# Performance work log

Measured on AMD Instinct MI355X. Metric: run time of the kernel, lower is better.

Reference implementation:

```python
import jax, jax.numpy as jnp
import numpy as np

EPS = 1e-08

def _compute_W(V, C, eps=EPS):
    # W = H_k ... H_1, applied sequentially as in the torch loop
    W = jnp.eye(C, dtype=V.dtype)
    def step(W, v):
        v = v / (jnp.linalg.norm(v) + eps)
        # H @ W = W - 2 v (v^T W)
        W = W - 2.0 * jnp.outer(v, v @ W)
        return W, None
    W, _ = jax.lax.scan(step, W, V)
    return W

def setup_inputs() -> dict:
    key = jax.random.key(0)
    k1, k2 = jax.random.split(key)
    x = jax.random.normal(k1, (16, 512, 64, 64), dtype=jnp.float32)
    V = jax.random.normal(k2, (32, 512), dtype=jnp.float32)
    return {"x": x, "V": V}

def reference(x, V):
    B, C, H, Wd = x.shape
    W = _compute_W(V, C)  # [C, C] orthogonal
    # 1x1 conv: out[b,o,h,w] = sum_c W[o,c] * x[b,c,h,w]
    return jnp.einsum('oc,bchw->bohw', W, x)
```

## Files before the change

### kernel.cpp

```cpp
#include <hip/hip_runtime.h>
#include <hip/hip_bf16.h>
#include <stdint.h>
#include <stddef.h>

#define HH_EPS 1e-8f

typedef __attribute__((ext_vector_type(8))) short short8;
typedef __attribute__((ext_vector_type(4))) float f32x4;

#define CDIM 512
#define SDIM 4096
#define BN 64
#define BK 32
#define NSTEP 16

__device__ __forceinline__ size_t wt_idx(int o, int c) {
    return (((size_t)(c >> 5) * 32 + (o >> 4)) * 64
            + (size_t)((c >> 3) & 3) * 16 + (o & 15)) * 8 + (c & 7);
}

__global__ void compute_w(const float* __restrict__ V,
                          __hip_bfloat16* __restrict__ Wt) {
    const int wave = threadIdx.x >> 6;
    const int lane = threadIdx.x & 63;
    const int jA = (blockIdx.x * 4 + wave) * 2;
    const int jB = jA + 1;
    const int ib = lane * 8;

    float wA[8], wB[8];
    #pragma unroll
    for (int r = 0; r < 8; r++) {
        wA[r] = (ib + r == jA) ? 1.0f : 0.0f;
        wB[r] = (ib + r == jB) ? 1.0f : 0.0f;
    }
    float4 c0 = *(const float4*)(V + ib);
    float4 c1 = *(const float4*)(V + ib + 4);

    for (int k = 0; k < 32; k++) {
        const float v[8] = {c0.x, c0.y, c0.z, c0.w, c1.x, c1.y, c1.z, c1.w};
        if (k < 31) {
            c0 = *(const float4*)(V + (size_t)(k + 1) * 512 + ib);
            c1 = *(const float4*)(V + (size_t)(k + 1) * 512 + ib + 4);
        }
        float dA = 0.0f, dB = 0.0f, ss = 0.0f;
        #pragma unroll
        for (int r = 0; r < 8; r++) {
            dA += v[r] * wA[r];
            dB += v[r] * wB[r];
            ss += v[r] * v[r];
        }
        #pragma unroll
        for (int off = 32; off > 0; off >>= 1) {
            dA += __shfl_xor(dA, off);
            dB += __shfl_xor(dB, off);
            ss += __shfl_xor(ss, off);
        }
        const float t = sqrtf(ss) + HH_EPS;
        const float scale = 2.0f / (t * t);
        const float tA = scale * dA, tB = scale * dB;
        #pragma unroll
        for (int r = 0; r < 8; r++) {
            wA[r] -= tA * v[r];
            wB[r] -= tB * v[r];
        }
    }
    #pragma unroll
    for (int r = 0; r < 8; r++) {
        Wt[wt_idx(ib + r, jA)] = __float2bfloat16(wA[r]);
        Wt[wt_idx(ib + r, jB)] = __float2bfloat16(wB[r]);
    }
}

__global__ __launch_bounds__(512, 2) void hh_gemm(
    const float* __restrict__ x,
    const __hip_bfloat16* __restrict__ Wt,
    float* __restrict__ out)
{
    const int tid  = threadIdx.x;
    const int wave = tid >> 6, lane = tid & 63;
    const int quad = lane >> 4, l16 = lane & 15;

    const int bid = blockIdx.x;
    const int b   = bid >> 6;
    const int nt  = bid & 63;
    const int n0  = nt * BN;

    const float* xb = x + (size_t)b * CDIM * SDIM + n0 + l16;
    const short8* wp = (const short8*)Wt + (size_t)wave * 4 * 64 + lane;

    f32x4 acc[4][4];
    #pragma unroll
    for (int mi = 0; mi < 4; mi++)
        #pragma unroll
        for (int oi = 0; oi < 4; oi++) {
            f32x4 z = {0.0f, 0.0f, 0.0f, 0.0f};
            acc[mi][oi] = z;
        }

    float  pfA[3][4][8];
    short8 wb[2][4];

    auto loadA = [&](int kt, int s) {
        const float* p = xb + (size_t)(kt * BK + quad * 8) * SDIM;
        #pragma unroll
        for (int mi = 0; mi < 4; mi++)
            #pragma unroll
            for (int e = 0; e < 8; e++)
                pfA[s][mi][e] = p[(size_t)e * SDIM + mi * 16];
    };
    auto loadW = [&](int kt, int s) {
        const short8* p = wp + (size_t)kt * 32 * 64;
        #pragma unroll
        for (int oi = 0; oi < 4; oi++)
            wb[s][oi] = p[oi * 64];
    };

    loadA(0, 0);
    loadW(0, 0);
    loadA(1, 1);

    #pragma unroll
    for (int kt = 0; kt < NSTEP; kt++) {
        if (kt + 1 < NSTEP) loadW(kt + 1, (kt + 1) & 1);
        if (kt + 2 < NSTEP) loadA(kt + 2, (kt + 2) % 3);
        const int s = kt % 3, w = kt & 1;
        #pragma unroll
        for (int mi = 0; mi < 4; mi++) {
            short8 afr;
            #pragma unroll
            for (int e = 0; e < 8; e++) {
                __hip_bfloat16 h = __float2bfloat16(pfA[s][mi][e]);
                afr[e] = *(const short*)&h;
            }
            #pragma unroll
            for (int oi = 0; oi < 4; oi++)
                acc[mi][oi] = __builtin_amdgcn_mfma_f32_16x16x32_bf16(
                    afr, wb[w][oi], acc[mi][oi], 0, 0, 0);
        }
    }

    float* ob = out + (size_t)b * CDIM * SDIM + n0;
    #pragma unroll
    for (int oi = 0; oi < 4; oi++) {
        const int o = wave * 64 + oi * 16 + l16;
        #pragma unroll
        for (int mi = 0; mi < 4; mi++)
            *(f32x4*)(ob + (size_t)o * SDIM + mi * 16 + quad * 4) = acc[mi][oi];
    }
}

extern "C" void kernel_launch(void* const* d_in, const int* in_sizes, int n_in,
                              void* d_out, int out_size, void* d_ws, size_t ws_size,
                              hipStream_t stream) {
    const float* x = (const float*)d_in[0];
    const float* V = (const float*)d_in[1];
    float* out = (float*)d_out;

    __hip_bfloat16* Wt = (__hip_bfloat16*)d_ws;

    compute_w<<<64, 256, 0, stream>>>(V, Wt);
    hh_gemm<<<1024, 512, 0, stream>>>(x, Wt, out);
}
```

Before: 316.0 us.

## Stage x tile in LDS once per block instead of per-wave redundant loads

Before, every wave loaded and converted the full x tile (64 columns by 32 k) from global memory on its own, so each block read it eight times. Now the block loads the tile cooperatively, with four floats per thread. It converts them to bf16 and writes them into a double-buffered LDS array, and each wave reads its MFMA fragments from there. Register use drops enough to raise launch bounds to 4 blocks per SM. The cost is a barrier per k-step, which adds synchronization and LDS traffic.

```diff
diff --git a/kernel.cpp b/kernel.cpp
--- a/kernel.cpp
+++ b/kernel.cpp
@@ -6,6 +6,7 @@
 #define HH_EPS 1e-8f
 
 typedef __attribute__((ext_vector_type(8))) short short8;
+typedef __attribute__((ext_vector_type(4))) short short4_t;
 typedef __attribute__((ext_vector_type(4))) float f32x4;
 
 #define CDIM 512
@@ -71,11 +72,18 @@
     }
 }
 
-__global__ __launch_bounds__(512, 2) void hh_gemm(
+__device__ __forceinline__ void lds_barrier() {
+    __builtin_amdgcn_s_waitcnt(0xC07F);
+    __builtin_amdgcn_s_barrier();
+}
+
+__global__ __launch_bounds__(512, 4) void hh_gemm(
     const float* __restrict__ x,
     const __hip_bfloat16* __restrict__ Wt,
     float* __restrict__ out)
 {
+    __shared__ __attribute__((aligned(16))) __hip_bfloat16 Bbuf[2][BN * BK];
+
     const int tid  = threadIdx.x;
     const int wave = tid >> 6, lane = tid & 63;
     const int quad = lane >> 4, l16 = lane & 15;
@@ -85,7 +93,12 @@
     const int nt  = bid & 63;
     const int n0  = nt * BN;
 
-    const float* xb = x + (size_t)b * CDIM * SDIM + n0 + l16;
+    const int bn = tid & 63;
+    const int kh = tid >> 6;
+    const int kq_s = kh >> 1, h_s = kh & 1;
+    const float* xp0 = x + (size_t)b * CDIM * SDIM
+                         + (size_t)(kq_s * 8 + h_s * 4) * SDIM + n0 + bn;
+
     const short8* wp = (const short8*)Wt + (size_t)wave * 4 * 64 + lane;
 
     f32x4 acc[4][4];
@@ -97,45 +110,54 @@
             acc[mi][oi] = z;
         }
 
-    float  pfA[3][4][8];
-    short8 wb[2][4];
+    float  pfB[2][4];
+    short8 wb[4];
 
-    auto loadA = [&](int kt, int s) {
-        const float* p = xb + (size_t)(kt * BK + quad * 8) * SDIM;
+    auto loadB = [&](int kt, int s) {
+        const float* p = xp0 + (size_t)kt * BK * SDIM;
         #pragma unroll
-        for (int mi = 0; mi < 4; mi++)
-            #pragma unroll
-            for (int e = 0; e < 8; e++)
-                pfA[s][mi][e] = p[(size_t)e * SDIM + mi * 16];
+        for (int j = 0; j < 4; j++) pfB[s][j] = p[(size_t)j * SDIM];
     };
-    auto loadW = [&](int kt, int s) {
+    auto writeB = [&](int buf, int s) {
+        short4_t pk;
+        #pragma unroll
+        for (int j = 0; j < 4; j++) {
+            __hip_bfloat16 h = __float2bfloat16(pfB[s][j]);
+            pk[j] = *(const short*)&h;
+        }
+        *(short4_t*)(&Bbuf[buf][(size_t)(bn >> 4) * 512
+                                + (size_t)(kq_s * 16 + (bn & 15)) * 8
+                                + h_s * 4]) = pk;
+    };
+    auto loadW = [&](int kt) {
         const short8* p = wp + (size_t)kt * 32 * 64;
         #pragma unroll
-        for (int oi = 0; oi < 4; oi++)
-            wb[s][oi] = p[oi * 64];
+        for (int oi = 0; oi < 4; oi++) wb[oi] = p[oi * 64];
     };
 
-    loadA(0, 0);
-    loadW(0, 0);
-    loadA(1, 1);
+    loadB(0, 0);
+    loadB(1, 1);
+    loadW(0);
+    writeB(0, 0);
+    lds_barrier();
 
     #pragma unroll
     for (int kt = 0; kt < NSTEP; kt++) {
-        if (kt + 1 < NSTEP) loadW(kt + 1, (kt + 1) & 1);
-        if (kt + 2 < NSTEP) loadA(kt + 2, (kt + 2) % 3);
-        const int s = kt % 3, w = kt & 1;
+        if (kt + 2 < NSTEP) loadB(kt + 2, kt & 1);
+        const int p = kt & 1;
         #pragma unroll
         for (int mi = 0; mi < 4; mi++) {
-            short8 afr;
-            #pragma unroll
-            for (int e = 0; e < 8; e++) {
-                __hip_bfloat16 h = __float2bfloat16(pfA[s][mi][e]);
-                afr[e] = *(const short*)&h;
-            }
+            const short8 afr =
+                *(const short8*)(&Bbuf[p][(size_t)(mi * 64 + lane) * 8]);
             #pragma unroll
             for (int oi = 0; oi < 4; oi++)
                 acc[mi][oi] = __builtin_amdgcn_mfma_f32_16x16x32_bf16(
-                    afr, wb[w][oi], acc[mi][oi], 0, 0, 0);
+                    afr, wb[oi], acc[mi][oi], 0, 0, 0);
+        }
+        if (kt + 1 < NSTEP) {
+            loadW(kt + 1);
+            writeB(p ^ 1, (kt + 1) & 1);
+            lds_barrier();
         }
     }
 
```

New measurement: 278.6 us. 1.13x faster.
